# Performance work log

Measured on AMD Instinct MI355X. Metric: run time of the kernel, lower is better.

The kernel has to match this reference:

```python
import jax, jax.numpy as jnp
import numpy as np

# Hardcoded 6-node part graph from the module (src, dst) pairs; PyG flows src->dst.
_EDGES = np.array([[0,1],[0,2],[0,3],[0,4],[0,5],[1,2],[1,3],[1,4],[1,5],[2,3],[2,4],[3,5],[4,5],[1,0],[2,0],[3,0],[4,0],[5,0],[2,1],[3,1],[4,1],[5,1],[3,2],[4,2],[5,3],[5,4]], dtype=np.int32)
SRC = jnp.asarray(_EDGES[:, 0])
DST = jnp.asarray(_EDGES[:, 1])
NUM_NODES = 6


def setup_inputs() -> dict:
    key = jax.random.key(0)
    k0, k1, k2 = jax.random.split(key, 3)
    C, B = 128, 32768
    x = jax.random.normal(k0, (NUM_NODES, B, C), dtype=jnp.float32)
    # SAGEConv weights: lin_l (aggregated neighbors, carries bias) and lin_r (root)
    W_l = jax.random.normal(k1, (2 * C, C), dtype=jnp.float32) / np.sqrt(C).astype(np.float32)
    W_r = jax.random.normal(k2, (2 * C, C), dtype=jnp.float32) / np.sqrt(C).astype(np.float32)
    b = jnp.zeros((2 * C,), dtype=jnp.float32)
    return {"x": x, "W_l": W_l, "W_r": W_r, "b": b}


def reference(x, W_l, W_r, b):
    # x: [N=6, B, C]
    # mean aggregation of source features at each destination node
    msg = x[SRC]                                                  # [E, B, C]
    agg = jax.ops.segment_sum(msg, DST, num_segments=NUM_NODES)   # [N, B, C]
    deg = jax.ops.segment_sum(jnp.ones_like(DST, dtype=x.dtype), DST, num_segments=NUM_NODES)
    agg = agg / deg[:, None, None]
    # SAGEConv: lin_l(agg) + lin_r(x), bias in lin_l
    y = jnp.einsum('nbc,oc->nbo', agg, W_l) + b + jnp.einsum('nbc,oc->nbo', x, W_r)
    y = jax.nn.gelu(y, approximate=False)                         # torch F.gelu = exact erf
    # Python cat-loop over nodes == concatenate the 6 node slices along features
    N, B, O = y.shape
    return jnp.transpose(y, (1, 0, 2)).reshape(B, N * O)          # [B, 6*2C]
```

## Files before the change

### kernel.cpp

```cpp
#include <hip/hip_runtime.h>
#include <hip/hip_bf16.h>

#define NB 32768
#define CD 128
#define NNODES 6
#define OUTW 1536
#define KW 256
#define GPB 4
#define NBLK (NB / 16 / GPB)

typedef __attribute__((ext_vector_type(8))) short short8;
typedef __attribute__((ext_vector_type(4))) short s16x4;
typedef __attribute__((ext_vector_type(4))) float f32x4;

static __device__ __forceinline__ short f2bf(float f) {
    union { __bf16 b; short s; } u;
    u.b = (__bf16)f;
    return u.s;
}

static __device__ __forceinline__ short8 pack8(f32x4 a, f32x4 b) {
    short8 p;
    #pragma unroll
    for (int j = 0; j < 4; ++j) { p[j] = f2bf(a[j]); p[4 + j] = f2bf(b[j]); }
    return p;
}

static __device__ __forceinline__ s16x4 pack4(f32x4 a) {
    s16x4 p;
    #pragma unroll
    for (int j = 0; j < 4; ++j) p[j] = f2bf(a[j]);
    return p;
}

__global__ void prep_w(const float* __restrict__ Wl, const float* __restrict__ Wr,
                       short* __restrict__ Wb) {
    const int i = (blockIdx.x * 256 + threadIdx.x) * 8;
    const int o = i >> 8;
    const int k = i & 255;
    const float* src = (k < 128) ? (Wl + o * CD + k) : (Wr + o * CD + (k - 128));
    *(short8*)(Wb + i) = pack8(*(const f32x4*)src, *(const f32x4*)(src + 4));
}

#define LIDX(p, r, k) ((((p) << 11) + ((r) << 7) + (k)) ^ (((r) & 7) << 3))

__global__ __launch_bounds__(512, 2)
void sage_v12(const float* __restrict__ x, const short* __restrict__ Wb,
              const float* __restrict__ bias, float* __restrict__ out) {
    __shared__ __align__(16) short A[2][10 * 16 * 128];

    const int t = threadIdx.x;
    const int r = t >> 5;
    const int c = t & 31;
    const int lane = t & 63;
    const int wv = t >> 6;
    const int lo = lane & 15;
    const int hi = lane >> 4;
    const int obase = wv * 32;
    const size_t rg0 = (size_t)blockIdx.x * GPB;

    f32x4 bias4[2];
    #pragma unroll
    for (int i = 0; i < 2; ++i)
        bias4[i] = *(const f32x4*)&bias[obase + i * 16 + hi * 4];

    auto loadConvert = [&](short* __restrict__ Ad, size_t rg) {
        const float* pb = x + (rg * 16 + r) * CD + c * 4;
        f32x4 v0 = *(const f32x4*)(pb + 0ull * (NB * CD));
        f32x4 v1 = *(const f32x4*)(pb + 1ull * (NB * CD));
        f32x4 v2 = *(const f32x4*)(pb + 2ull * (NB * CD));
        f32x4 v3 = *(const f32x4*)(pb + 3ull * (NB * CD));
        f32x4 v4 = *(const f32x4*)(pb + 4ull * (NB * CD));
        f32x4 v5 = *(const f32x4*)(pb + 5ull * (NB * CD));
        f32x4 S01 = v0 + v1, S25 = v2 + v5, S34 = v3 + v4;
        f32x4 T = S01 + S25 + S34;
        const int k = c * 4;
        *(s16x4*)&Ad[LIDX(0, r, k)] = pack4((T - v0) * 0.2f);
        *(s16x4*)&Ad[LIDX(1, r, k)] = pack4((T - v1) * 0.2f);
        *(s16x4*)&Ad[LIDX(2, r, k)] = pack4((S01 + S34) * 0.25f);
        *(s16x4*)&Ad[LIDX(3, r, k)] = pack4((S01 + S25) * 0.25f);
        *(s16x4*)&Ad[LIDX(4, r, k)] = pack4(v0);
        *(s16x4*)&Ad[LIDX(5, r, k)] = pack4(v1);
        *(s16x4*)&Ad[LIDX(6, r, k)] = pack4(v2);
        *(s16x4*)&Ad[LIDX(7, r, k)] = pack4(v3);
        *(s16x4*)&Ad[LIDX(8, r, k)] = pack4(v4);
        *(s16x4*)&Ad[LIDX(9, r, k)] = pack4(v5);
    };

    auto pairMFMA = [&](const short* __restrict__ Ab, int pa0, int pa1,
                        int px0, int px1, f32x4 acc[2][2]) {
        #pragma unroll
        for (int n = 0; n < 2; ++n)
            #pragma unroll
            for (int i = 0; i < 2; ++i) acc[n][i] = (f32x4){0.f, 0.f, 0.f, 0.f};
        #pragma unroll
        for (int m = 0; m < 4; ++m) {
            const int kk = m * 32 + hi * 8;
            short8 fa0 = *(const short8*)&Ab[LIDX(pa0, lo, kk)];
            short8 fa1 = *(const short8*)&Ab[LIDX(pa1, lo, kk)];
            short8 fx0 = *(const short8*)&Ab[LIDX(px0, lo, kk)];
            short8 fx1 = *(const short8*)&Ab[LIDX(px1, lo, kk)];
            #pragma unroll
            for (int i = 0; i < 2; ++i) {
                const int o = obase + i * 16 + lo;
                short8 wa = *(const short8*)&Wb[o * KW + kk];
                short8 wx = *(const short8*)&Wb[o * KW + 128 + kk];
                acc[0][i] = __builtin_amdgcn_mfma_f32_16x16x32_bf16(wa, fa0, acc[0][i], 0, 0, 0);
                acc[1][i] = __builtin_amdgcn_mfma_f32_16x16x32_bf16(wa, fa1, acc[1][i], 0, 0, 0);
                acc[0][i] = __builtin_amdgcn_mfma_f32_16x16x32_bf16(wx, fx0, acc[0][i], 0, 0, 0);
                acc[1][i] = __builtin_amdgcn_mfma_f32_16x16x32_bf16(wx, fx1, acc[1][i], 0, 0, 0);
            }
        }
    };

    auto storePair = [&](int n0, int n1, f32x4 acc[2][2], size_t orow) {
        #pragma unroll
        for (int w = 0; w < 2; ++w) {
            const int node = w ? n1 : n0;
            #pragma unroll
            for (int i = 0; i < 2; ++i) {
                const int ocol = obase + i * 16 + hi * 4;
                f32x4 v = acc[w][i] + bias4[i];
                f32x4 g;
                #pragma unroll
                for (int j = 0; j < 4; ++j) {
                    const float s = v[j] * (0.7978845608f + 0.0356774081f * v[j] * v[j]);
                    const float rr = __builtin_amdgcn_exp2f(-2.885390082f * s);
                    g[j] = v[j] * __builtin_amdgcn_rcpf(1.0f + rr);
                }
                *(f32x4*)&out[orow * OUTW + node * 256 + ocol] = g;
            }
        }
    };

    loadConvert(&A[0][0], rg0);
    __syncthreads();

    f32x4 accH[2][2];
    size_t prevRow = 0;

    #pragma unroll 1
    for (int it = 0; it < GPB; ++it) {
        if (it) __syncthreads();
        const short* Ab = &A[it & 1][0];
        const size_t orow = (rg0 + it) * 16 + lo;

        if (it) storePair(3, 4, accH, prevRow);

        f32x4 acc[2][2];
        pairMFMA(Ab, 0, 1, 4, 5, acc);
        storePair(0, 1, acc, orow);
        pairMFMA(Ab, 2, 2, 6, 9, acc);
        storePair(2, 5, acc, orow);
        pairMFMA(Ab, 3, 3, 7, 8, accH);
        prevRow = orow;

        if (it + 1 < GPB) loadConvert(&A[(it + 1) & 1][0], rg0 + it + 1);
    }
    storePair(3, 4, accH, prevRow);
}

extern "C" void kernel_launch(void* const* d_in, const int* in_sizes, int n_in,
                              void* d_out, int out_size, void* d_ws, size_t ws_size,
                              hipStream_t stream) {
    const float* x  = (const float*)d_in[0];
    const float* Wl = (const float*)d_in[1];
    const float* Wr = (const float*)d_in[2];
    const float* b  = (const float*)d_in[3];
    float* out = (float*)d_out;
    short* Wb = (short*)d_ws;

    prep_w<<<dim3(32), dim3(256), 0, stream>>>(Wl, Wr, Wb);
    sage_v12<<<dim3(NBLK), dim3(512), 0, stream>>>(x, Wb, b, out);
}
```

Baseline: 87.85 us.

## Stage x into LDS asynchronously and keep weight fragments in registers

Input rows are now fetched with global_load_lds into a raw fp32 LDS staging buffer one group ahead, then converted to bf16 from LDS, instead of loading from global straight into registers. The goal is to hide global-memory latency behind the MFMA work. Weight fragments are loaded into registers once per block instead of being re-read from global memory inside every MFMA loop. Groups per block double and launch bounds drop to one block per CU. The extra LDS buffer and the larger register footprint cut occupancy, which may hurt latency hiding for this memory-bound kernel.

```diff
diff --git a/kernel.cpp b/kernel.cpp
--- a/kernel.cpp
+++ b/kernel.cpp
@@ -6,7 +6,7 @@
 #define NNODES 6
 #define OUTW 1536
 #define KW 256
-#define GPB 4
+#define GPB 8
 #define NBLK (NB / 16 / GPB)
 
 typedef __attribute__((ext_vector_type(8))) short short8;
@@ -44,9 +44,10 @@
 
 #define LIDX(p, r, k) ((((p) << 11) + ((r) << 7) + (k)) ^ (((r) & 7) << 3))
 
-__global__ __launch_bounds__(512, 2)
-void sage_v12(const float* __restrict__ x, const short* __restrict__ Wb,
+__global__ __launch_bounds__(512, 1)
+void sage_v13(const float* __restrict__ x, const short* __restrict__ Wb,
               const float* __restrict__ bias, float* __restrict__ out) {
+    __shared__ __align__(16) float raw[NNODES * 16 * 128];
     __shared__ __align__(16) short A[2][10 * 16 * 128];
 
     const int t = threadIdx.x;
@@ -64,14 +65,36 @@
     for (int i = 0; i < 2; ++i)
         bias4[i] = *(const f32x4*)&bias[obase + i * 16 + hi * 4];
 
-    auto loadConvert = [&](short* __restrict__ Ad, size_t rg) {
-        const float* pb = x + (rg * 16 + r) * CD + c * 4;
-        f32x4 v0 = *(const f32x4*)(pb + 0ull * (NB * CD));
-        f32x4 v1 = *(const f32x4*)(pb + 1ull * (NB * CD));
-        f32x4 v2 = *(const f32x4*)(pb + 2ull * (NB * CD));
-        f32x4 v3 = *(const f32x4*)(pb + 3ull * (NB * CD));
-        f32x4 v4 = *(const f32x4*)(pb + 4ull * (NB * CD));
-        f32x4 v5 = *(const f32x4*)(pb + 5ull * (NB * CD));
+    short8 wfa[4][2], wfx[4][2];
+    #pragma unroll
+    for (int m = 0; m < 4; ++m)
+        #pragma unroll
+        for (int i = 0; i < 2; ++i) {
+            const int kk = m * 32 + hi * 8;
+            const int o = obase + i * 16 + lo;
+            wfa[m][i] = *(const short8*)&Wb[o * KW + kk];
+            wfx[m][i] = *(const short8*)&Wb[o * KW + 128 + kk];
+        }
+
+    auto stage = [&](size_t rg) {
+        const float* gp = x + (rg * 16 + r) * CD + c * 4;
+        #pragma unroll
+        for (int s = 0; s < NNODES; ++s) {
+            __builtin_amdgcn_global_load_lds(
+                (const __attribute__((address_space(1))) void*)(gp + (size_t)s * (NB * CD)),
+                (__attribute__((address_space(3))) void*)&raw[s * 2048 + wv * 256],
+                16, 0, 0);
+        }
+    };
+
+    auto convert = [&](short* __restrict__ Ad) {
+        const int base = r * 128 + c * 4;
+        f32x4 v0 = *(const f32x4*)&raw[0 * 2048 + base];
+        f32x4 v1 = *(const f32x4*)&raw[1 * 2048 + base];
+        f32x4 v2 = *(const f32x4*)&raw[2 * 2048 + base];
+        f32x4 v3 = *(const f32x4*)&raw[3 * 2048 + base];
+        f32x4 v4 = *(const f32x4*)&raw[4 * 2048 + base];
+        f32x4 v5 = *(const f32x4*)&raw[5 * 2048 + base];
         f32x4 S01 = v0 + v1, S25 = v2 + v5, S34 = v3 + v4;
         f32x4 T = S01 + S25 + S34;
         const int k = c * 4;
@@ -102,13 +125,10 @@
             short8 fx1 = *(const short8*)&Ab[LIDX(px1, lo, kk)];
             #pragma unroll
             for (int i = 0; i < 2; ++i) {
-                const int o = obase + i * 16 + lo;
-                short8 wa = *(const short8*)&Wb[o * KW + kk];
-                short8 wx = *(const short8*)&Wb[o * KW + 128 + kk];
-                acc[0][i] = __builtin_amdgcn_mfma_f32_16x16x32_bf16(wa, fa0, acc[0][i], 0, 0, 0);
-                acc[1][i] = __builtin_amdgcn_mfma_f32_16x16x32_bf16(wa, fa1, acc[1][i], 0, 0, 0);
-                acc[0][i] = __builtin_amdgcn_mfma_f32_16x16x32_bf16(wx, fx0, acc[0][i], 0, 0, 0);
-                acc[1][i] = __builtin_amdgcn_mfma_f32_16x16x32_bf16(wx, fx1, acc[1][i], 0, 0, 0);
+                acc[0][i] = __builtin_amdgcn_mfma_f32_16x16x32_bf16(wfa[m][i], fa0, acc[0][i], 0, 0, 0);
+                acc[1][i] = __builtin_amdgcn_mfma_f32_16x16x32_bf16(wfa[m][i], fa1, acc[1][i], 0, 0, 0);
+                acc[0][i] = __builtin_amdgcn_mfma_f32_16x16x32_bf16(wfx[m][i], fx0, acc[0][i], 0, 0, 0);
+                acc[1][i] = __builtin_amdgcn_mfma_f32_16x16x32_bf16(wfx[m][i], fx1, acc[1][i], 0, 0, 0);
             }
         }
     };
@@ -133,7 +153,10 @@
         }
     };
 
-    loadConvert(&A[0][0], rg0);
+    stage(rg0);
+    asm volatile("s_waitcnt vmcnt(0)" ::: "memory");
+    convert(&A[0][0]);
+    if (GPB > 1) stage(rg0 + 1);
     __syncthreads();
 
     f32x4 accH[2][2];
@@ -141,7 +164,6 @@
 
     #pragma unroll 1
     for (int it = 0; it < GPB; ++it) {
-        if (it) __syncthreads();
         const short* Ab = &A[it & 1][0];
         const size_t orow = (rg0 + it) * 16 + lo;
 
@@ -155,7 +177,12 @@
         pairMFMA(Ab, 3, 3, 7, 8, accH);
         prevRow = orow;
 
-        if (it + 1 < GPB) loadConvert(&A[(it + 1) & 1][0], rg0 + it + 1);
+        if (it + 1 < GPB) {
+            asm volatile("s_waitcnt vmcnt(0)" ::: "memory");
+            convert(&A[(it + 1) & 1][0]);
+            if (it + 2 < GPB) stage(rg0 + it + 2);
+        }
+        __syncthreads();
     }
     storePair(3, 4, accH, prevRow);
 }
@@ -171,5 +198,5 @@
     short* Wb = (short*)d_ws;
 
     prep_w<<<dim3(32), dim3(256), 0, stream>>>(Wl, Wr, Wb);
-    sage_v12<<<dim3(NBLK), dim3(512), 0, stream>>>(x, Wb, b, out);
-}
+    sage_v13<<<dim3(NBLK), dim3(512), 0, stream>>>(x, Wb, b, out);
+}
```

Measured after the change: 86.96 us. Within noise of the previous version (-1.0%).
